# Kernel tuning notes

Hardware: AMD Instinct MI355X
Metric: run time of the kernel (lower is better)

## Reference

```python
import jax, jax.numpy as jnp
import numpy as np

D_MODEL = 1024
N_HEADS = 16
HEAD = D_MODEL // N_HEADS
B, T = 4, 2048


def setup_inputs() -> dict:
    key = jax.random.key(0)
    ks = jax.random.split(key, 8)
    s = 0.02
    return {
        "x_enc": jax.random.normal(ks[0], (B, T, D_MODEL), dtype=jnp.float32),
        "x_dec": jax.random.normal(ks[1], (B, T, D_MODEL), dtype=jnp.float32),
        "mask": jnp.zeros((B, T, T), dtype=jnp.float32),
        "Wq": jax.random.normal(ks[2], (D_MODEL, D_MODEL), dtype=jnp.float32) * s,
        "bq": jnp.zeros((D_MODEL,), dtype=jnp.float32),
        "Wkv": jax.random.normal(ks[3], (D_MODEL, 2 * D_MODEL), dtype=jnp.float32) * s,
        "bkv": jnp.zeros((2 * D_MODEL,), dtype=jnp.float32),
        "Wo": jax.random.normal(ks[4], (D_MODEL, D_MODEL), dtype=jnp.float32) * s,
        "bo": jnp.zeros((D_MODEL,), dtype=jnp.float32),
    }


def reference(x_enc, x_dec, mask, Wq, bq, Wkv, bkv, Wo, bo):
    b, t, c = x_enc.shape
    # projections
    kv = x_enc @ Wkv + bkv                     # [B,T,2C]
    q = x_dec @ Wq + bq                        # [B,T,C]
    # split heads (replicates torch reshape of interleaved kv)
    kv = kv.reshape(b, t, N_HEADS, 2 * HEAD).transpose(0, 2, 1, 3)  # [B,H,T,2hs]
    q = q.reshape(b, t, N_HEADS, HEAD).transpose(0, 2, 1, 3)        # [B,H,T,hs]
    k, v = kv[..., :HEAD], kv[..., HEAD:]
    # attention
    scores = jnp.einsum("bhqd,bhkd->bhqk", q, k) / np.sqrt(HEAD).astype(np.float32)
    scores = scores + mask[:, None, :, :]      # additive mask, broadcast over heads
    attn = jax.nn.softmax(scores, axis=-1)
    res = jnp.einsum("bhqk,bhkd->bhqd", attn, v)   # [B,H,T,hs]
    res = res.transpose(0, 2, 1, 3).reshape(b, t, c)
    return res @ Wo + bo
```

## Files before the change

### kernel.cpp

```cpp
#include <hip/hip_runtime.h>
#include <hip/hip_bf16.h>
#include <math.h>


#define D_MODEL 1024
#define NH      16
#define HEAD    64
#define BATCH   4
#define SEQ     2048
#define QB      256

#define LOG2E   1.44269504088896f

typedef unsigned int   u32;
typedef unsigned short u16;
typedef __attribute__((ext_vector_type(8))) short s16x8;
typedef __attribute__((ext_vector_type(4))) float f32x4;
typedef __attribute__((ext_vector_type(4))) unsigned int u32v4;

__device__ __forceinline__ u16 tobf(float f) {
    u32 u = __builtin_bit_cast(u32, f);
    return (u16)((u + 0x7fffu + ((u >> 16) & 1u)) >> 16);
}
__device__ __forceinline__ float frombf(u16 u) {
    return __builtin_bit_cast(float, (u32)u << 16);
}
__device__ __forceinline__ u32 cvtpk(float a, float b) {
    u32 r;
    asm("v_cvt_pk_bf16_f32 %0, %1, %2" : "=v"(r) : "v"(a), "v"(b));
    return r;
}
__device__ __forceinline__ float fexp2(float x) {
    float r;
    asm("v_exp_f32 %0, %1" : "=v"(r) : "v"(x));
    return r;
}

__device__ __forceinline__ void gl_lds16(const void* g, void* l) {
    __builtin_amdgcn_global_load_lds(
        (const __attribute__((address_space(1))) u32*)g,
        (__attribute__((address_space(3))) u32*)l, 16, 0, 0);
}

__global__ __launch_bounds__(256) void cast_bf16_2(
    const float* __restrict__ in0, const float* __restrict__ in1,
    u16* __restrict__ out, int n)
{
    const float* in = blockIdx.y ? in1 : in0;
    u16* o = out + (size_t)blockIdx.y * n;
    int i = (blockIdx.x * 256 + threadIdx.x) * 4;
    if (i < n) {
        float4 v = *(const float4*)(in + i);
        ushort4 ov = make_ushort4(tobf(v.x), tobf(v.y), tobf(v.z), tobf(v.w));
        *(ushort4*)(o + i) = ov;
    }
}

__global__ __launch_bounds__(256) void mask_prep(
    const float* __restrict__ mask, u16* __restrict__ mp)
{
    const size_t gt = (size_t)blockIdx.x * 256 + threadIdx.x;
    const int l = (int)(gt & 63);
    const size_t tile = gt >> 6;
    const int kt = (int)(tile & 127);
    const size_t bq = tile >> 7;
    const int qt = (int)(bq & 127);
    const int b  = (int)(bq >> 7);
    const int q15 = l & 15, quad = l >> 4;
    const int q = qt*16 + q15;
    const int k = (kt >> 2)*64 + ((kt >> 1) & 1)*32 + (kt & 1)*4 + quad*8;
    float4 v = *(const float4*)&mask[((size_t)(b*SEQ + q))*SEQ + k];
    ushort4 o = make_ushort4(tobf(v.x * LOG2E), tobf(v.y * LOG2E),
                             tobf(v.z * LOG2E), tobf(v.w * LOG2E));
    *(ushort4*)&mp[tile*256 + (size_t)l*4] = o;
}

__global__ __launch_bounds__(256) void transpose_cast4(
    const float* __restrict__ Wq,  u16* __restrict__ wqT,
    const float* __restrict__ Wkv, u16* __restrict__ wkvT,
    const float* __restrict__ Wo,  u16* __restrict__ woT)
{
    const int K = D_MODEL;
    const int z = blockIdx.z;
    const float* W = (z == 0) ? Wq : (z == 3) ? Wo : Wkv;
    u16* WT       = (z == 0) ? wqT : (z == 3) ? woT : wkvT;
    const int N   = (z == 1 || z == 2) ? 2*D_MODEL : D_MODEL;
    const int nb  = (z == 2) ? D_MODEL : 0;

    __shared__ __align__(16) float tile[32][33];
    const int n0 = nb + blockIdx.x * 32, k0 = blockIdx.y * 32;
    const int r = threadIdx.x >> 3, c4 = (threadIdx.x & 7) * 4;
    float4 v = *(const float4*)&W[(size_t)(k0 + r) * N + n0 + c4];
    tile[r][c4] = v.x; tile[r][c4+1] = v.y; tile[r][c4+2] = v.z; tile[r][c4+3] = v.w;
    __syncthreads();
    ushort4 o = make_ushort4(tobf(tile[c4+0][r]), tobf(tile[c4+1][r]),
                             tobf(tile[c4+2][r]), tobf(tile[c4+3][r]));
    *(ushort4*)&WT[(size_t)(n0 + r) * K + k0 + c4] = o;
}

__device__ __forceinline__ void store_out(u16* p, float v)  { *p = tobf(v); }
__device__ __forceinline__ void store_out(float* p, float v){ *p = v; }

template <typename OT>
__global__ __launch_bounds__(256) void gemm_bt(
    const u16* __restrict__ A, const u16* __restrict__ Bt,
    const float* __restrict__ bias, OT* __restrict__ C,
    int N, int K, float out_scale)
{
    __shared__ __align__(16) u16 As[3][128 * 32];
    __shared__ __align__(16) u16 Bs[3][128 * 32];
    const int t = threadIdx.x;
    const int w = t >> 6, l = t & 63;
    const int lane15 = l & 15, quad = l >> 4;
    const int m0 = blockIdx.y * 128, n0 = blockIdx.x * 128;
    const int wm = (w >> 1) * 64, wn = (w & 1) * 64;
    const int lr = l >> 2, lk = (l & 3) * 8;

    auto stage = [&](int k0, int bufi) {
        #pragma unroll
        for (int i = 0; i < 2; ++i) {
            const int chunk = w * 2 + i;
            gl_lds16(A  + (size_t)(m0 + chunk*16 + lr) * K + k0 + lk,
                     &As[bufi][chunk * 512]);
            gl_lds16(Bt + (size_t)(n0 + chunk*16 + lr) * K + k0 + lk,
                     &Bs[bufi][chunk * 512]);
        }
    };
    auto compute = [&](int cur, f32x4 (*acc)[4]) {
        s16x8 af[4], bfr[4];
        #pragma unroll
        for (int i2 = 0; i2 < 4; ++i2)
            af[i2] = *(const s16x8*)&As[cur][(wm + i2*16 + lane15) * 32 + quad * 8];
        #pragma unroll
        for (int j = 0; j < 4; ++j)
            bfr[j] = *(const s16x8*)&Bs[cur][(wn + j*16 + lane15) * 32 + quad * 8];
        #pragma unroll
        for (int i2 = 0; i2 < 4; ++i2)
            #pragma unroll
            for (int j = 0; j < 4; ++j)
                acc[i2][j] = __builtin_amdgcn_mfma_f32_16x16x32_bf16(
                    af[i2], bfr[j], acc[i2][j], 0, 0, 0);
    };

    f32x4 acc[4][4] = {};
    const int nb = K >> 5;
    stage(0, 0);
    stage(32, 1);

    for (int i = 0; i < nb - 1; ++i) {
        const int cur = i % 3;
        asm volatile("s_waitcnt vmcnt(4)" ::: "memory");
        __builtin_amdgcn_sched_barrier(0);
        __builtin_amdgcn_s_barrier();
        if (i + 2 < nb) stage((i + 2) << 5, (i + 2) % 3);
        compute(cur, acc);
    }
    {
        const int cur = (nb - 1) % 3;
        asm volatile("s_waitcnt vmcnt(0)" ::: "memory");
        __builtin_amdgcn_sched_barrier(0);
        __builtin_amdgcn_s_barrier();
        compute(cur, acc);
    }

    #pragma unroll
    for (int j = 0; j < 4; ++j) {
        const int col = n0 + wn + j*16 + lane15;
        const float bv = bias[col];
        #pragma unroll
        for (int i = 0; i < 4; ++i)
            #pragma unroll
            for (int r = 0; r < 4; ++r) {
                const int row = m0 + wm + i*16 + quad*4 + r;
                store_out(C + (size_t)row * N + col, (acc[i][j][r] + bv) * out_scale);
            }
    }
}

__global__ __launch_bounds__(256) void gemm_kv(
    const u16* __restrict__ A, const u16* __restrict__ Bt,
    const float* __restrict__ bias, u16* __restrict__ kvb,
    u16* __restrict__ vtb)
{
    const int N = 2 * D_MODEL, K = D_MODEL;
    __shared__ __align__(16) u16 As[2][128 * 32];
    __shared__ __align__(16) u16 Bs[2][128 * 32];
    const int t = threadIdx.x;
    const int w = t >> 6, l = t & 63;
    const int lane15 = l & 15, quad = l >> 4;
    const int m0 = blockIdx.y * 128, n0 = blockIdx.x * 128;
    const int wm = (w >> 1) * 64, wn = (w & 1) * 64;
    const int lr = l >> 2, lk = (l & 3) * 8;

    auto stage = [&](int k0, int bufi) {
        #pragma unroll
        for (int i = 0; i < 2; ++i) {
            const int chunk = w * 2 + i;
            gl_lds16(A  + (size_t)(m0 + chunk*16 + lr) * K + k0 + lk,
                     &As[bufi][chunk * 512]);
            gl_lds16(Bt + (size_t)(n0 + chunk*16 + lr) * K + k0 + lk,
                     &Bs[bufi][chunk * 512]);
        }
    };

    f32x4 acc[4][4] = {};
    const int nb = K >> 5;
    stage(0, 0);

    for (int i = 0; i < nb; ++i) {
        const int cur = i & 1;
        __syncthreads();
        if (i + 1 < nb) stage((i + 1) << 5, cur ^ 1);
        s16x8 af[4], bfr[4];
        #pragma unroll
        for (int i2 = 0; i2 < 4; ++i2)
            af[i2] = *(const s16x8*)&As[cur][(wm + i2*16 + lane15) * 32 + quad * 8];
        #pragma unroll
        for (int j = 0; j < 4; ++j)
            bfr[j] = *(const s16x8*)&Bs[cur][(wn + j*16 + lane15) * 32 + quad * 8];
        #pragma unroll
        for (int i2 = 0; i2 < 4; ++i2)
            #pragma unroll
            for (int j = 0; j < 4; ++j)
                acc[i2][j] = __builtin_amdgcn_mfma_f32_16x16x32_bf16(
                    af[i2], bfr[j], acc[i2][j], 0, 0, 0);
    }

    if (wn == 0) {
        #pragma unroll
        for (int j = 0; j < 4; ++j) {
            const int col = n0 + j*16 + lane15;
            const float bv = bias[col];
            #pragma unroll
            for (int i = 0; i < 4; ++i)
                #pragma unroll
                for (int r = 0; r < 4; ++r) {
                    const int row = m0 + wm + i*16 + quad*4 + r;
                    kvb[(size_t)row * N + col] = tobf(acc[i][j][r] + bv);
                }
        }
    } else {
        const int bh = (m0 >> 11) * NH + (n0 >> 7);
        #pragma unroll
        for (int j = 0; j < 4; ++j) {
            const int d = j*16 + lane15;
            const float bv = bias[n0 + 64 + d];
            #pragma unroll
            for (int i = 0; i < 4; ++i) {
                const int row = m0 + wm + i*16 + quad*4;
                const int tt = row & (SEQ - 1);
                u16* p = vtb + ((size_t)bh*64 + d)*SEQ + tt;
                *(uint2*)p = make_uint2(cvtpk(acc[i][j][0]+bv, acc[i][j][1]+bv),
                                        cvtpk(acc[i][j][2]+bv, acc[i][j][3]+bv));
            }
        }
    }
}

__global__ __launch_bounds__(512, 4) void attn_mfma(
    const u16* __restrict__ qb, const u16* __restrict__ kvb,
    const u16* __restrict__ vt, const u16* __restrict__ mp,
    u16* __restrict__ resb)
{
    __shared__ __align__(16) u16 sm[4*4096];
    const int t = threadIdx.x;
    const int w = t >> 6, l = t & 63;
    const int lane15 = l & 15, quad = l >> 4;
    const int h  = blockIdx.x;
    const int q0 = blockIdx.y * QB;
    const int b  = blockIdx.z;
    const int bh = b * NH + h;
    const int lr4 = l >> 2;
    const int lc8 = (((l & 3) ^ (lr4 & 3)) * 8);
    const int cq  = (quad ^ (lane15 & 3)) * 8;
    const int kprow = (lr4 >> 2)*8 + (lr4 & 3);

    s16x8 aq0[2], aq1[2];
    #pragma unroll
    for (int s = 0; s < 2; ++s) {
        const u16* qrow = qb + (size_t)(b*SEQ + q0 + w*32 + s*16 + lane15) * D_MODEL + h*HEAD;
        aq0[s] = *(const s16x8*)(qrow + quad*8);
        aq1[s] = *(const s16x8*)(qrow + 32 + quad*8);
    }
    const u16* mrow[2];
    #pragma unroll
    for (int s = 0; s < 2; ++s)
        mrow[s] = mp + (((size_t)b*128 + (q0>>4) + w*2 + s) * 128) * 256 + (size_t)l*4;

    auto stage = [&](int k0s, int bf) {
        const int hh = w & 1, rr = w >> 1;
        const int krow = (rr >> 1)*32 + (rr & 1)*4 + kprow;
        const u16* kg = kvb + (size_t)(b*SEQ + k0s + krow) * (2*D_MODEL)
                            + h*128 + hh*32 + lc8;
        gl_lds16(kg, sm + bf*4096 + hh*2048 + rr*512);
        const u16* vg = vt + (size_t)(bh*64 + rr*16 + lr4) * SEQ
                           + k0s + hh*32 + lc8;
        gl_lds16(vg, sm + 8192 + bf*4096 + hh*2048 + rr*512);
    };

    f32x4 o_acc[2][4] = {};
    f32x4 l_acc[2] = {};
    ushort4 mreg[2][4];
    s16x8 vones;
    #pragma unroll
    for (int i = 0; i < 8; ++i) vones[i] = (short)0x3F80;

    stage(0, 0);
    #pragma unroll
    for (int s = 0; s < 2; ++s)
        #pragma unroll
        for (int nt = 0; nt < 4; ++nt)
            mreg[s][nt] = *(const ushort4*)(mrow[s] + (size_t)nt * 256);

    for (int it = 0; it < SEQ/64; ++it) {
        const int k0 = it * 64;
        const int bf = it & 1;
        __syncthreads();
        if (it + 1 < SEQ/64)
            stage(k0 + 64, bf ^ 1);

        f32x4 sv[2][4];
        #pragma unroll
        for (int s = 0; s < 2; ++s)
            #pragma unroll
            for (int nt = 0; nt < 4; ++nt) {
                sv[s][nt][0] = frombf(mreg[s][nt].x); sv[s][nt][1] = frombf(mreg[s][nt].y);
                sv[s][nt][2] = frombf(mreg[s][nt].z); sv[s][nt][3] = frombf(mreg[s][nt].w);
            }
        __builtin_amdgcn_s_setprio(1);
        #pragma unroll
        for (int nt = 0; nt < 4; ++nt) {
            s16x8 kf0 = *(const s16x8*)(sm + bf*4096 +        (nt*16 + lane15)*32 + cq);
            s16x8 kf1 = *(const s16x8*)(sm + bf*4096 + 2048 + (nt*16 + lane15)*32 + cq);
            #pragma unroll
            for (int s = 0; s < 2; ++s) {
                sv[s][nt] = __builtin_amdgcn_mfma_f32_16x16x32_bf16(kf0, aq0[s], sv[s][nt], 0, 0, 0);
                sv[s][nt] = __builtin_amdgcn_mfma_f32_16x16x32_bf16(kf1, aq1[s], sv[s][nt], 0, 0, 0);
            }
        }
        __builtin_amdgcn_s_setprio(0);

        if (it + 1 < SEQ/64) {
            #pragma unroll
            for (int s = 0; s < 2; ++s)
                #pragma unroll
                for (int nt = 0; nt < 4; ++nt)
                    mreg[s][nt] = *(const ushort4*)(mrow[s] + ((size_t)((k0+64)>>4) + nt) * 256);
        }

        s16x8 pf[2][2];
        #pragma unroll
        for (int s = 0; s < 2; ++s)
            #pragma unroll
            for (int hf = 0; hf < 2; ++hf) {
                u32v4 pk;
                pk[0] = cvtpk(fexp2(sv[s][2*hf][0]),   fexp2(sv[s][2*hf][1]));
                pk[1] = cvtpk(fexp2(sv[s][2*hf][2]),   fexp2(sv[s][2*hf][3]));
                pk[2] = cvtpk(fexp2(sv[s][2*hf+1][0]), fexp2(sv[s][2*hf+1][1]));
                pk[3] = cvtpk(fexp2(sv[s][2*hf+1][2]), fexp2(sv[s][2*hf+1][3]));
                pf[s][hf] = __builtin_bit_cast(s16x8, pk);
            }

        __builtin_amdgcn_s_setprio(1);
        #pragma unroll
        for (int s = 0; s < 2; ++s) {
            l_acc[s] = __builtin_amdgcn_mfma_f32_16x16x32_bf16(vones, pf[s][0], l_acc[s], 0, 0, 0);
            l_acc[s] = __builtin_amdgcn_mfma_f32_16x16x32_bf16(vones, pf[s][1], l_acc[s], 0, 0, 0);
        }
        #pragma unroll
        for (int dt = 0; dt < 4; ++dt) {
            s16x8 vf0 = *(const s16x8*)(sm + 8192 + bf*4096 +        (dt*16 + lane15)*32 + cq);
            s16x8 vf1 = *(const s16x8*)(sm + 8192 + bf*4096 + 2048 + (dt*16 + lane15)*32 + cq);
            #pragma unroll
            for (int s = 0; s < 2; ++s) {
                o_acc[s][dt] = __builtin_amdgcn_mfma_f32_16x16x32_bf16(vf0, pf[s][0], o_acc[s][dt], 0, 0, 0);
                o_acc[s][dt] = __builtin_amdgcn_mfma_f32_16x16x32_bf16(vf1, pf[s][1], o_acc[s][dt], 0, 0, 0);
            }
        }
        __builtin_amdgcn_s_setprio(0);
    }

    __syncthreads();
    #pragma unroll
    for (int s = 0; s < 2; ++s) {
        const float inv = 1.f / l_acc[s][0];
        u16* orow = &sm[(w*32 + s*16 + lane15) * 64];
        #pragma unroll
        for (int dt = 0; dt < 4; ++dt) {
            *(uint2*)&orow[dt*16 + quad*4] = make_uint2(
                cvtpk(o_acc[s][dt][0]*inv, o_acc[s][dt][1]*inv),
                cvtpk(o_acc[s][dt][2]*inv, o_acc[s][dt][3]*inv));
        }
    }
    __syncthreads();
    {
        const int tr = t >> 1, tc = (t & 1) * 32;
        u16* o = resb + (size_t)(b*SEQ + q0 + tr) * D_MODEL + h*HEAD + tc;
        #pragma unroll
        for (int j = 0; j < 4; ++j)
            *(uint4*)(o + j*8) = *(const uint4*)&sm[tr*64 + tc + j*8];
    }
}

extern "C" void kernel_launch(void* const* d_in, const int* in_sizes, int n_in,
                              void* d_out, int out_size, void* d_ws, size_t ws_size,
                              hipStream_t stream) {
    const float* x_enc = (const float*)d_in[0];
    const float* x_dec = (const float*)d_in[1];
    const float* mask  = (const float*)d_in[2];
    const float* Wq    = (const float*)d_in[3];
    const float* bq    = (const float*)d_in[4];
    const float* Wkv   = (const float*)d_in[5];
    const float* bkv   = (const float*)d_in[6];
    const float* Wo    = (const float*)d_in[7];
    const float* bo    = (const float*)d_in[8];
    float* out = (float*)d_out;

    const int M = BATCH * SEQ;
    u16* xe   = (u16*)d_ws;
    u16* xd   = xe   + (size_t)M * D_MODEL;
    u16* wqT  = xd   + (size_t)M * D_MODEL;
    u16* wkvT = wqT  + (size_t)D_MODEL * D_MODEL;
    u16* woT  = wkvT + (size_t)2*D_MODEL*D_MODEL;
    u16* qbuf = woT  + (size_t)D_MODEL * D_MODEL;
    u16* kvb  = qbuf + (size_t)M * D_MODEL;
    u16* vtb  = kvb  + (size_t)M * 2 * D_MODEL;
    u16* resb = vtb  + (size_t)BATCH*NH*HEAD*SEQ;
    u16* mpk  = xe;

    const int NX = M * D_MODEL;
    cast_bf16_2<<<dim3(NX/1024, 2), 256, 0, stream>>>(x_enc, x_dec, xe, NX);
    transpose_cast4<<<dim3(32, 32, 4), 256, 0, stream>>>(
        Wq, wqT, Wkv, wkvT, Wo, woT);

    gemm_kv<<<dim3(2*D_MODEL/128, M/128), 256, 0, stream>>>(
        xe, wkvT, bkv, kvb, vtb);
    gemm_bt<u16><<<dim3(D_MODEL/128, M/128), 256, 0, stream>>>(
        xd, wqT, bq, qbuf, D_MODEL, D_MODEL, 0.125f * LOG2E);
    mask_prep<<<(BATCH*128*128*64)/256, 256, 0, stream>>>(mask, mpk);
    attn_mfma<<<dim3(NH, SEQ/QB, BATCH), 512, 0, stream>>>(
        qbuf, kvb, vtb, mpk, resb);
    gemm_bt<float><<<dim3(D_MODEL/128, M/128), 256, 0, stream>>>(
        resb, woT, bo, out, D_MODEL, D_MODEL, 1.0f);
}
```

Baseline: 382.3 us.

## Read fp32 mask directly in attention, add XCD swizzle, simplify GEMM pipeline

Removes the mask_prep kernel and has the attention kernel load the fp32 mask directly, applying the LOG2E scale in registers. This saves one launch plus the bf16 mask write and re-read, but every one of the 16 head blocks now reads fp32 mask data, which doubles per-read bytes compared with bf16. Both GEMMs also gain an XCD-aware block swizzle to improve L2 locality. gemm_bt drops from a 3-stage vmcnt-tuned pipeline to a simpler 2-stage double buffer with __syncthreads, which may lose some load/compute overlap.

```diff
diff --git a/kernel.cpp b/kernel.cpp
--- a/kernel.cpp
+++ b/kernel.cpp
@@ -56,25 +56,6 @@
     }
 }
 
-__global__ __launch_bounds__(256) void mask_prep(
-    const float* __restrict__ mask, u16* __restrict__ mp)
-{
-    const size_t gt = (size_t)blockIdx.x * 256 + threadIdx.x;
-    const int l = (int)(gt & 63);
-    const size_t tile = gt >> 6;
-    const int kt = (int)(tile & 127);
-    const size_t bq = tile >> 7;
-    const int qt = (int)(bq & 127);
-    const int b  = (int)(bq >> 7);
-    const int q15 = l & 15, quad = l >> 4;
-    const int q = qt*16 + q15;
-    const int k = (kt >> 2)*64 + ((kt >> 1) & 1)*32 + (kt & 1)*4 + quad*8;
-    float4 v = *(const float4*)&mask[((size_t)(b*SEQ + q))*SEQ + k];
-    ushort4 o = make_ushort4(tobf(v.x * LOG2E), tobf(v.y * LOG2E),
-                             tobf(v.z * LOG2E), tobf(v.w * LOG2E));
-    *(ushort4*)&mp[tile*256 + (size_t)l*4] = o;
-}
-
 __global__ __launch_bounds__(256) void transpose_cast4(
     const float* __restrict__ Wq,  u16* __restrict__ wqT,
     const float* __restrict__ Wkv, u16* __restrict__ wkvT,
@@ -98,6 +79,14 @@
     *(ushort4*)&WT[(size_t)(n0 + r) * K + k0 + c4] = o;
 }
 
+__device__ __forceinline__ void xcd_swz(int& bx, int& by) {
+    const int gx = gridDim.x;
+    const int nwg = gx * gridDim.y;
+    const int orig = by * gx + bx;
+    const int swz = (orig & 7) * (nwg >> 3) + (orig >> 3);
+    bx = swz % gx; by = swz / gx;
+}
+
 __device__ __forceinline__ void store_out(u16* p, float v)  { *p = tobf(v); }
 __device__ __forceinline__ void store_out(float* p, float v){ *p = v; }
 
@@ -107,12 +96,14 @@
     const float* __restrict__ bias, OT* __restrict__ C,
     int N, int K, float out_scale)
 {
-    __shared__ __align__(16) u16 As[3][128 * 32];
-    __shared__ __align__(16) u16 Bs[3][128 * 32];
+    __shared__ __align__(16) u16 As[2][128 * 32];
+    __shared__ __align__(16) u16 Bs[2][128 * 32];
     const int t = threadIdx.x;
     const int w = t >> 6, l = t & 63;
     const int lane15 = l & 15, quad = l >> 4;
-    const int m0 = blockIdx.y * 128, n0 = blockIdx.x * 128;
+    int bx = blockIdx.x, by = blockIdx.y;
+    xcd_swz(bx, by);
+    const int m0 = by * 128, n0 = bx * 128;
     const int wm = (w >> 1) * 64, wn = (w & 1) * 64;
     const int lr = l >> 2, lk = (l & 3) * 8;
 
@@ -126,7 +117,15 @@
                      &Bs[bufi][chunk * 512]);
         }
     };
-    auto compute = [&](int cur, f32x4 (*acc)[4]) {
+
+    f32x4 acc[4][4] = {};
+    const int nb = K >> 5;
+    stage(0, 0);
+
+    for (int i = 0; i < nb; ++i) {
+        const int cur = i & 1;
+        __syncthreads();
+        if (i + 1 < nb) stage((i + 1) << 5, cur ^ 1);
         s16x8 af[4], bfr[4];
         #pragma unroll
         for (int i2 = 0; i2 < 4; ++i2)
@@ -140,29 +139,7 @@
             for (int j = 0; j < 4; ++j)
                 acc[i2][j] = __builtin_amdgcn_mfma_f32_16x16x32_bf16(
                     af[i2], bfr[j], acc[i2][j], 0, 0, 0);
-    };
-
-    f32x4 acc[4][4] = {};
-    const int nb = K >> 5;
-    stage(0, 0);
-    stage(32, 1);
-
-    for (int i = 0; i < nb - 1; ++i) {
-        const int cur = i % 3;
-        asm volatile("s_waitcnt vmcnt(4)" ::: "memory");
-        __builtin_amdgcn_sched_barrier(0);
-        __builtin_amdgcn_s_barrier();
-        if (i + 2 < nb) stage((i + 2) << 5, (i + 2) % 3);
-        compute(cur, acc);
-    }
-    {
-        const int cur = (nb - 1) % 3;
-        asm volatile("s_waitcnt vmcnt(0)" ::: "memory");
-        __builtin_amdgcn_sched_barrier(0);
-        __builtin_amdgcn_s_barrier();
-        compute(cur, acc);
-    }
-
+    }
     #pragma unroll
     for (int j = 0; j < 4; ++j) {
         const int col = n0 + wn + j*16 + lane15;
@@ -188,7 +165,9 @@
     const int t = threadIdx.x;
     const int w = t >> 6, l = t & 63;
     const int lane15 = l & 15, quad = l >> 4;
-    const int m0 = blockIdx.y * 128, n0 = blockIdx.x * 128;
+    int bx = blockIdx.x, by = blockIdx.y;
+    xcd_swz(bx, by);
+    const int m0 = by * 128, n0 = bx * 128;
     const int wm = (w >> 1) * 64, wn = (w & 1) * 64;
     const int lr = l >> 2, lk = (l & 3) * 8;
 
@@ -259,7 +238,7 @@
 
 __global__ __launch_bounds__(512, 4) void attn_mfma(
     const u16* __restrict__ qb, const u16* __restrict__ kvb,
-    const u16* __restrict__ vt, const u16* __restrict__ mp,
+    const u16* __restrict__ vt, const float* __restrict__ mask,
     u16* __restrict__ resb)
 {
     __shared__ __align__(16) u16 sm[4*4096];
@@ -282,10 +261,11 @@
         aq0[s] = *(const s16x8*)(qrow + quad*8);
         aq1[s] = *(const s16x8*)(qrow + 32 + quad*8);
     }
-    const u16* mrow[2];
+    const float* mrow[2];
     #pragma unroll
     for (int s = 0; s < 2; ++s)
-        mrow[s] = mp + (((size_t)b*128 + (q0>>4) + w*2 + s) * 128) * 256 + (size_t)l*4;
+        mrow[s] = mask + (size_t)(b*SEQ + q0 + w*32 + s*16 + lane15) * SEQ + quad*8;
+    const int koff[4] = {0, 4, 32, 36};
 
     auto stage = [&](int k0s, int bf) {
         const int hh = w & 1, rr = w >> 1;
@@ -300,7 +280,7 @@
 
     f32x4 o_acc[2][4] = {};
     f32x4 l_acc[2] = {};
-    ushort4 mreg[2][4];
+    float4 mreg[2][4];
     s16x8 vones;
     #pragma unroll
     for (int i = 0; i < 8; ++i) vones[i] = (short)0x3F80;
@@ -310,7 +290,7 @@
     for (int s = 0; s < 2; ++s)
         #pragma unroll
         for (int nt = 0; nt < 4; ++nt)
-            mreg[s][nt] = *(const ushort4*)(mrow[s] + (size_t)nt * 256);
+            mreg[s][nt] = *(const float4*)(mrow[s] + koff[nt]);
 
     for (int it = 0; it < SEQ/64; ++it) {
         const int k0 = it * 64;
@@ -324,8 +304,10 @@
         for (int s = 0; s < 2; ++s)
             #pragma unroll
             for (int nt = 0; nt < 4; ++nt) {
-                sv[s][nt][0] = frombf(mreg[s][nt].x); sv[s][nt][1] = frombf(mreg[s][nt].y);
-                sv[s][nt][2] = frombf(mreg[s][nt].z); sv[s][nt][3] = frombf(mreg[s][nt].w);
+                sv[s][nt][0] = mreg[s][nt].x * LOG2E;
+                sv[s][nt][1] = mreg[s][nt].y * LOG2E;
+                sv[s][nt][2] = mreg[s][nt].z * LOG2E;
+                sv[s][nt][3] = mreg[s][nt].w * LOG2E;
             }
         __builtin_amdgcn_s_setprio(1);
         #pragma unroll
@@ -345,7 +327,7 @@
             for (int s = 0; s < 2; ++s)
                 #pragma unroll
                 for (int nt = 0; nt < 4; ++nt)
-                    mreg[s][nt] = *(const ushort4*)(mrow[s] + ((size_t)((k0+64)>>4) + nt) * 256);
+                    mreg[s][nt] = *(const float4*)(mrow[s] + (k0 + 64) + koff[nt]);
         }
 
         s16x8 pf[2][2];
@@ -426,7 +408,6 @@
     u16* kvb  = qbuf + (size_t)M * D_MODEL;
     u16* vtb  = kvb  + (size_t)M * 2 * D_MODEL;
     u16* resb = vtb  + (size_t)BATCH*NH*HEAD*SEQ;
-    u16* mpk  = xe;
 
     const int NX = M * D_MODEL;
     cast_bf16_2<<<dim3(NX/1024, 2), 256, 0, stream>>>(x_enc, x_dec, xe, NX);
@@ -437,9 +418,8 @@
         xe, wkvT, bkv, kvb, vtb);
     gemm_bt<u16><<<dim3(D_MODEL/128, M/128), 256, 0, stream>>>(
         xd, wqT, bq, qbuf, D_MODEL, D_MODEL, 0.125f * LOG2E);
-    mask_prep<<<(BATCH*128*128*64)/256, 256, 0, stream>>>(mask, mpk);
     attn_mfma<<<dim3(NH, SEQ/QB, BATCH), 512, 0, stream>>>(
-        qbuf, kvb, vtb, mpk, resb);
+        qbuf, kvb, vtb, mask, resb);
     gemm_bt<float><<<dim3(D_MODEL/128, M/128), 256, 0, stream>>>(
         resb, woT, bo, out, D_MODEL, D_MODEL, 1.0f);
 }
```

Result: slower. 442.1 us (+15.6%).
